# Kernel optimization log

Hardware: AMD Instinct MI355X
Metric: run time of the kernel (lower is better)

## Reference

```python
import jax, jax.numpy as jnp
import numpy as np

B, MAX_ATOM, N_FEAT = 64, 128, 128
DENSITY = 0.1  # fraction of nonzero off-diagonal Laplacian entries


def setup_inputs() -> dict:
    key = jax.random.key(0)
    k1, k2, k3, k4 = jax.random.split(key, 4)
    node_features = jax.random.normal(k1, (B, MAX_ATOM, N_FEAT), dtype=jnp.float32)
    u = jax.random.uniform(k2, (B, MAX_ATOM, MAX_ATOM))
    vals = jax.random.normal(k3, (B, MAX_ATOM, MAX_ATOM), dtype=jnp.float32)
    lap = jnp.where(u < DENSITY, vals, 0.0)
    eye = jnp.eye(MAX_ATOM, dtype=jnp.float32)[None]
    laplacian = lap * (1.0 - eye) + eye  # diagonal always nonzero (degree term)
    # per-molecule true atom counts in [1, MAX_ATOM]
    n_atoms = jax.random.randint(k4, (B,), 1, MAX_ATOM + 1, dtype=jnp.int32)
    mol_slice = jnp.stack([n_atoms, jnp.full((B,), N_FEAT, jnp.int32)], axis=1)
    l_slice = jnp.stack([n_atoms, n_atoms], axis=1)
    return {"node_features": node_features, "laplacian": laplacian,
            "mol_slice": mol_slice, "l_slice": l_slice}


def _pool_one(x, L, n):
    # x: [A, F], L: [A, A], n: scalar valid atom count
    A = x.shape[0]
    valid = jnp.arange(A) < n                             # [A]
    mask = (L != 0) & valid[None, :] & valid[:, None]     # [A, A] neighbor mask
    # masked max over neighbors j of x[j]
    neigh = jnp.where(mask[:, :, None], x[None, :, :], -jnp.inf)  # [A, A, F]
    pooled = jnp.max(neigh, axis=1)                       # [A, F]
    has_nb = jnp.any(mask, axis=1)                        # [A]
    pooled = jnp.where(has_nb[:, None], pooled, x)        # fallback to self
    return jnp.where(valid[:, None], pooled, 0.0)         # zero-pad to max_atom


def reference(node_features, laplacian, mol_slice, l_slice):
    n_atoms = mol_slice[:, 0]
    return jax.vmap(_pool_one)(node_features, laplacian, n_atoms)
```

## Files before the change

### kernel.cpp

```cpp
#include <hip/hip_runtime.h>
#include <math.h>


#define MAX_ATOM 128
#define N_FEAT 128

__global__ __launch_bounds__(N_FEAT) void GraphPoolMol_kernel(
    const float* __restrict__ x,
    const float* __restrict__ L,
    const int* __restrict__ mol_slice,
    float* __restrict__ out)
{
    const int i = blockIdx.x;
    const int b = blockIdx.y;
    const int f = threadIdx.x;

    const int n = mol_slice[b * 2];

    const size_t base = ((size_t)b * MAX_ATOM + i) * N_FEAT;
    float* orow = out + base;

    if (i >= n) {
        orow[f] = 0.0f;
        return;
    }

    const float* __restrict__ xb   = x + (size_t)b * MAX_ATOM * N_FEAT;
    const float* __restrict__ Lrow = L + ((size_t)b * MAX_ATOM + i) * MAX_ATOM;

    __shared__ int nbr[MAX_ATOM];
    __shared__ int cnt;
    if (f == 0) cnt = 0;
    __syncthreads();

    float lv = (f < n) ? Lrow[f] : 0.0f;
    if (lv != 0.0f) {
        int pos = atomicAdd(&cnt, 1);
        nbr[pos] = f;
    }
    __syncthreads();

    const int m = cnt;
    float acc = -INFINITY;
    for (int k = 0; k < m; ++k) {
        const int j = nbr[k];
        acc = fmaxf(acc, xb[(size_t)j * N_FEAT + f]);
    }
    if (m == 0) acc = xb[(size_t)i * N_FEAT + f];
    orow[f] = acc;
}

extern "C" void kernel_launch(void* const* d_in, const int* in_sizes, int n_in,
                              void* d_out, int out_size, void* d_ws, size_t ws_size,
                              hipStream_t stream) {
    const float* x   = (const float*)d_in[0];
    const float* L   = (const float*)d_in[1];
    const int* mol   = (const int*)d_in[2];
    float* out = (float*)d_out;

    dim3 grid(MAX_ATOM, 64);
    dim3 block(N_FEAT);
    GraphPoolMol_kernel<<<grid, block, 0, stream>>>(x, L, mol, out);
}
```

Before: 66.51 us.

## Map one wavefront per atom row using ballot neighbor masks and float2 loads

Each 64-lane wavefront now handles one output row, with four rows per 256-thread block. Neighbor sets come from wave ballots over float2-loaded Laplacian entries, replacing the shared-memory atomic list and both __syncthreads. Each lane loads and reduces two features through float2 accesses. The cost is two serial ctz loops that split even and odd neighbors, and the loss of neighbor-order locality.

New measurement: 67.35 us. Within noise of the previous version (+1.2%).

```diff
diff --git a/kernel.cpp b/kernel.cpp
--- a/kernel.cpp
+++ b/kernel.cpp
@@ -4,50 +4,65 @@
 
 #define MAX_ATOM 128
 #define N_FEAT 128
+#define NBATCH 64
 
-__global__ __launch_bounds__(N_FEAT) void GraphPoolMol_kernel(
+__global__ __launch_bounds__(256) void GraphPoolMol_kernel(
     const float* __restrict__ x,
     const float* __restrict__ L,
     const int* __restrict__ mol_slice,
     float* __restrict__ out)
 {
-    const int i = blockIdx.x;
-    const int b = blockIdx.y;
-    const int f = threadIdx.x;
+    const int lane = threadIdx.x & 63;
+    const int wav  = threadIdx.x >> 6;
+    const int i    = blockIdx.x * 4 + wav;
+    const int b    = blockIdx.y;
 
     const int n = mol_slice[b * 2];
 
-    const size_t base = ((size_t)b * MAX_ATOM + i) * N_FEAT;
-    float* orow = out + base;
+    float2* orow = (float2*)(out + ((size_t)b * MAX_ATOM + i) * N_FEAT);
 
     if (i >= n) {
-        orow[f] = 0.0f;
+        orow[lane] = make_float2(0.0f, 0.0f);
         return;
     }
 
-    const float* __restrict__ xb   = x + (size_t)b * MAX_ATOM * N_FEAT;
-    const float* __restrict__ Lrow = L + ((size_t)b * MAX_ATOM + i) * MAX_ATOM;
+    const float* __restrict__ xb = x + (size_t)b * MAX_ATOM * N_FEAT;
+    const float2* __restrict__ Lrow2 =
+        (const float2*)(L + ((size_t)b * MAX_ATOM + i) * MAX_ATOM);
 
-    __shared__ int nbr[MAX_ATOM];
-    __shared__ int cnt;
-    if (f == 0) cnt = 0;
-    __syncthreads();
+    const float2 lv = Lrow2[lane];
+    const int j0 = lane * 2;
+    const int j1 = j0 + 1;
+    const unsigned long long m0 = __ballot((lv.x != 0.0f) && (j0 < n));
+    const unsigned long long m1 = __ballot((lv.y != 0.0f) && (j1 < n));
 
-    float lv = (f < n) ? Lrow[f] : 0.0f;
-    if (lv != 0.0f) {
-        int pos = atomicAdd(&cnt, 1);
-        nbr[pos] = f;
+    float2 acc = make_float2(-INFINITY, -INFINITY);
+
+    unsigned long long mm = m0;
+    while (mm) {
+        const int l = __builtin_ctzll(mm);
+        mm &= mm - 1;
+        const float2* xr = (const float2*)(xb + (size_t)(2 * l) * N_FEAT);
+        const float2 v = xr[lane];
+        acc.x = fmaxf(acc.x, v.x);
+        acc.y = fmaxf(acc.y, v.y);
     }
-    __syncthreads();
+    mm = m1;
+    while (mm) {
+        const int l = __builtin_ctzll(mm);
+        mm &= mm - 1;
+        const float2* xr = (const float2*)(xb + (size_t)(2 * l + 1) * N_FEAT);
+        const float2 v = xr[lane];
+        acc.x = fmaxf(acc.x, v.x);
+        acc.y = fmaxf(acc.y, v.y);
+    }
 
-    const int m = cnt;
-    float acc = -INFINITY;
-    for (int k = 0; k < m; ++k) {
-        const int j = nbr[k];
-        acc = fmaxf(acc, xb[(size_t)j * N_FEAT + f]);
+    if ((m0 | m1) == 0ull) {
+        const float2* xr = (const float2*)(xb + (size_t)i * N_FEAT);
+        acc = xr[lane];
     }
-    if (m == 0) acc = xb[(size_t)i * N_FEAT + f];
-    orow[f] = acc;
+
+    orow[lane] = acc;
 }
 
 extern "C" void kernel_launch(void* const* d_in, const int* in_sizes, int n_in,
@@ -58,7 +73,7 @@
     const int* mol   = (const int*)d_in[2];
     float* out = (float*)d_out;
 
-    dim3 grid(MAX_ATOM, 64);
-    dim3 block(N_FEAT);
+    dim3 grid(MAX_ATOM / 4, NBATCH);
+    dim3 block(256);
     GraphPoolMol_kernel<<<grid, block, 0, stream>>>(x, L, mol, out);
 }
```
